# Optimization experiments

Hardware: AMD Instinct MI355X
Metric: run time of the kernel (lower is better)

## Reference

```python
import jax, jax.numpy as jnp
import numpy as np

DELTA = 0.0  # default `delta` arg of forward


def _features(voxels, clust_ids, num_clusters):
    # voxels: [N,3] float, clust_ids: [N] int in [0, C)
    n = voxels.shape[0]
    seg = lambda x: jax.ops.segment_sum(x, clust_ids, num_segments=num_clusters)
    counts = seg(jnp.ones((n,), voxels.dtype))                     # [C] cluster sizes
    safe_cnt = jnp.maximum(counts, 1.0)
    center = seg(voxels) / safe_cnt[:, None]                       # [C,3] per-cluster mean
    xc = voxels - center[clust_ids]                                # [N,3] centered voxels
    cov = seg(xc[:, :, None] * xc[:, None, :])                     # [C,3,3] = x^T x per cluster
    w, v = jnp.linalg.eigh(cov)                                    # eigvals ascending (== torch.eig + argsort)
    w2 = w[:, 2]
    dirwt = jnp.where(w2 == 0, 0.0, 1.0 - w[:, 1] / jnp.where(w2 == 0, 1.0, w2))
    wd = w + DELTA
    denom = jnp.where(wd[:, 2] == 0, 1.0, wd[:, 2])
    wn = wd / denom[:, None]                                       # w normalized by largest
    eye = jnp.eye(3, dtype=voxels.dtype)
    B = (1.0 - DELTA) * jnp.einsum('cij,cj,ckj->cik', v, wn, v) + DELTA * eye  # [C,3,3]
    v0 = v[:, :, 2]                                                # [C,3] principal axis
    x0 = jnp.sum(xc * v0[clust_ids], axis=-1)                      # [N] projection on v0
    xp0 = xc - x0[:, None] * v0[clust_ids]                         # [N,3] residual
    np0 = jnp.linalg.norm(xp0, axis=1)                             # [N]
    sc = seg(x0 * np0)                                             # [C] sign score
    v0 = jnp.where((sc < 0)[:, None], -v0, v0) * dirwt[:, None]
    # len(c) < 2 branch: center = the voxel itself (mean handles it), B = delta*I, v0 = 0
    small = counts < 2.0
    B = jnp.where(small[:, None, None], DELTA * eye, B)
    v0 = jnp.where(small[:, None], 0.0, v0)
    return jnp.concatenate([center, B.reshape(num_clusters, 9), v0, counts[:, None]], axis=1)  # [C,16]


def setup_inputs() -> dict:
    key = jax.random.key(0)
    k1, k2 = jax.random.split(key)
    n, c = 4000000, 4096
    data = jax.random.normal(k1, (n, 5), dtype=jnp.float32)
    clust_ids = jax.random.randint(k2, (n,), 0, c)
    return {"data": data, "clust_ids": clust_ids, "num_clusters": c}


def reference(data, clust_ids, num_clusters):
    voxels = data[:, :3].astype(jnp.float32)
    return _features(voxels, clust_ids, num_clusters)
```

## Files before the change

### kernel.cpp

```cpp
#include <hip/hip_runtime.h>
#include <math.h>

#define NC 4096
#define OVCAP 131072
#define CAP1 8520

__device__ __forceinline__ int xcd_id() {
    return (int)__builtin_amdgcn_s_getreg(20 | (0 << 6) | ((4 - 1) << 11));
}

__device__ __forceinline__ void solve_cluster(const float mom[10], float* o,
                                              float4* pcv, float4* pvv) {
    float cntf = mom[0];
    double dn  = (double)cntf;
    double inv = 1.0 / fmax(dn, 1.0);
    double cx = mom[1] * inv, cy = mom[2] * inv, cz = mom[3] * inv;

    double a00 = (double)mom[4] - dn * cx * cx;
    double a01 = (double)mom[5] - dn * cx * cy;
    double a02 = (double)mom[6] - dn * cx * cz;
    double a11 = (double)mom[7] - dn * cy * cy;
    double a12 = (double)mom[8] - dn * cy * cz;
    double a22 = (double)mom[9] - dn * cz * cz;

    double q  = (a00 + a11 + a22) / 3.0;
    double p1 = a01 * a01 + a02 * a02 + a12 * a12;
    double b00 = a00 - q, b11 = a11 - q, b22 = a22 - q;
    double p2 = b00 * b00 + b11 * b11 + b22 * b22 + 2.0 * p1;
    double w0, w1, w2;
    if (!(p2 > 0.0)) {
        w0 = w1 = w2 = q;
    } else {
        double p  = sqrt(p2 / 6.0);
        double ip = 1.0 / p;
        double c00 = b00 * ip, c01 = a01 * ip, c02 = a02 * ip;
        double c11 = b11 * ip, c12 = a12 * ip, c22 = b22 * ip;
        double detB = c00 * (c11 * c22 - c12 * c12)
                    - c01 * (c01 * c22 - c12 * c02)
                    + c02 * (c01 * c12 - c11 * c02);
        double r = fmin(1.0, fmax(-1.0, detB * 0.5));
        double phi = acos(r) / 3.0;
        w2 = q + 2.0 * p * cos(phi);
        w0 = q + 2.0 * p * cos(phi + 2.0943951023931953);
        w1 = 3.0 * q - w2 - w0;
    }

    double denom = (w2 == 0.0) ? 1.0 : w2;
    double dirwt = (w2 == 0.0) ? 0.0 : (1.0 - w1 / w2);

    double C00 = a00 - w1, C11 = a11 - w1, C22 = a22 - w1;
    double D00 = a00 - w0, D11 = a11 - w0, D22 = a22 - w0;
    double M00 = C00 * D00 + a01 * a01 + a02 * a02;
    double M10 = a01 * D00 + C11 * a01 + a12 * a02;
    double M20 = a02 * D00 + a12 * a01 + C22 * a02;
    double M01 = C00 * a01 + a01 * D11 + a02 * a12;
    double M11 = a01 * a01 + C11 * D11 + a12 * a12;
    double M21 = a02 * a01 + a12 * D11 + C22 * a12;
    double M02 = C00 * a02 + a01 * a12 + a02 * D22;
    double M12 = a01 * a02 + C11 * a12 + a12 * D22;
    double M22 = a02 * a02 + a12 * a12 + C22 * D22;
    double n0 = M00 * M00 + M10 * M10 + M20 * M20;
    double n1 = M01 * M01 + M11 * M11 + M21 * M21;
    double n2 = M02 * M02 + M12 * M12 + M22 * M22;
    double vx, vy, vz, nn;
    if (n0 >= n1 && n0 >= n2) { vx = M00; vy = M10; vz = M20; nn = n0; }
    else if (n1 >= n2)        { vx = M01; vy = M11; vz = M21; nn = n1; }
    else                      { vx = M02; vy = M12; vz = M22; nn = n2; }
    if (nn > 1e-300) {
        double rn = 1.0 / sqrt(nn);
        vx *= rn; vy *= rn; vz *= rn;
    } else {
        vx = vy = vz = 0.0;
    }

    bool small = cntf < 2.0f;
    float bscale = small ? 0.0f : (float)(1.0 / denom);

    o[0]  = (float)cx;
    o[1]  = (float)cy;
    o[2]  = (float)cz;
    o[3]  = (float)a00 * bscale;
    o[4]  = (float)a01 * bscale;
    o[5]  = (float)a02 * bscale;
    o[6]  = (float)a01 * bscale;
    o[7]  = (float)a11 * bscale;
    o[8]  = (float)a12 * bscale;
    o[9]  = (float)a02 * bscale;
    o[10] = (float)a12 * bscale;
    o[11] = (float)a22 * bscale;
    o[15] = cntf;

    *pcv = make_float4((float)cx, (float)cy, (float)cz, (float)dirwt);
    *pvv = make_float4((float)vx, (float)vy, (float)vz, cntf);
}

__device__ __forceinline__ void ov_spill(float4 d, int id, float4* ov, int* novf,
                                         float* gmom) {
    int ovi = atomicAdd(novf, 1);
    if (ovi < OVCAP) ov[ovi] = d;
    atomicAdd(&gmom[0 * NC + id], 1.0f);
    atomicAdd(&gmom[1 * NC + id], d.x);
    atomicAdd(&gmom[2 * NC + id], d.y);
    atomicAdd(&gmom[3 * NC + id], d.z);
    atomicAdd(&gmom[4 * NC + id], d.x * d.x);
    atomicAdd(&gmom[5 * NC + id], d.x * d.y);
    atomicAdd(&gmom[6 * NC + id], d.x * d.z);
    atomicAdd(&gmom[7 * NC + id], d.y * d.y);
    atomicAdd(&gmom[8 * NC + id], d.y * d.z);
    atomicAdd(&gmom[9 * NC + id], d.z * d.z);
}

__global__ __launch_bounds__(256) void k_p1(const float* __restrict__ data,
                                            const int* __restrict__ ids,
                                            float4* __restrict__ P1,
                                            int* __restrict__ cnt1,
                                            float4* __restrict__ ov,
                                            int* __restrict__ novf,
                                            float* __restrict__ gmom, int n) {
    __shared__ float4 srt[2048];
    __shared__ int h64[64], boff[64], bglob[64];
    int tid = threadIdx.x, lane = tid & 63;
    int xcd = xcd_id() & 7;
    int ntiles = (n + 2047) >> 11;
    for (int t = blockIdx.x; t < ntiles; t += gridDim.x) {
        int vbase = t << 11;
        if (tid < 64) h64[tid] = 0;
        __syncthreads();
        float vx[8], vy[8], vz[8];
        int vid[8], vrk[8];
#pragma unroll
        for (int s = 0; s < 8; s++) {
            int v = vbase + (s << 8) + tid;
            if (v < n) {
                vx[s] = data[v * 5 + 0];
                vy[s] = data[v * 5 + 1];
                vz[s] = data[v * 5 + 2];
                int id = ids[v];
                vid[s] = id;
                vrk[s] = atomicAdd(&h64[id >> 6], 1);
            } else vid[s] = -1;
        }
        __syncthreads();
        if (tid < 64) {
            int c0 = h64[tid], sc = c0;
            for (int off = 1; off < 64; off <<= 1) {
                int u = __shfl_up(sc, off);
                if (lane >= off) sc += u;
            }
            boff[tid] = sc - c0;
            bglob[tid] = atomicAdd(&cnt1[((tid << 3) + xcd) << 4], c0);
        }
        __syncthreads();
#pragma unroll
        for (int s = 0; s < 8; s++)
            if (vid[s] >= 0)
                srt[boff[vid[s] >> 6] + vrk[s]] =
                    make_float4(vx[s], vy[s], vz[s], __int_as_float(vid[s]));
        __syncthreads();
        int tot = n - vbase;
        tot = tot > 2048 ? 2048 : tot;
        for (int i = tid; i < tot; i += 256) {
            float4 d = srt[i];
            int id = __float_as_int(d.w);
            int b = id >> 6;
            int ofs = bglob[b] + (i - boff[b]);
            if (ofs < CAP1)
                P1[(size_t)((b << 3) + xcd) * CAP1 + ofs] = d;
            else
                ov_spill(d, id, ov, novf, gmom);
        }
        __syncthreads();
    }
}

__global__ __launch_bounds__(256) void k_mom(const float4* __restrict__ P1,
                                             const int* __restrict__ cnt1,
                                             float* __restrict__ gmom) {
    __shared__ float4 srt[2048];
    __shared__ int h64[64], boff[64];
    int tid = threadIdx.x, lane = tid & 63, w4 = tid >> 6;
    int xcd = blockIdx.x & 7;
    int rest = blockIdx.x >> 3;
    int bucket = rest & 63;
    int q = rest >> 6;
    int sub = (bucket << 3) + xcd;

    int m1c = cnt1[sub << 4];
    m1c = m1c > CAP1 ? CAP1 : m1c;
    int start = (int)(((long long)m1c * q) >> 1);
    int end   = (int)(((long long)m1c * (q + 1)) >> 1);
    size_t sbase = (size_t)sub * CAP1;

    float creg = 0.0f;
    float m1 = 0, m2 = 0, m3 = 0, m4 = 0, m5 = 0, m6 = 0, m7 = 0, m8 = 0, m9 = 0;

    for (int tb = start; tb < end; tb += 2048) {
        if (tid < 64) h64[tid] = 0;
        __syncthreads();
        float4 vd[8];
        int vcid[8], vrk[8];
#pragma unroll
        for (int s = 0; s < 8; s++) {
            int i = tb + (s << 8) + tid;
            if (i < end) {
                float4 d = P1[sbase + i];
                int cid = __float_as_int(d.w) & 63;
                vd[s] = d; vcid[s] = cid;
                vrk[s] = atomicAdd(&h64[cid], 1);
            } else vcid[s] = -1;
        }
        __syncthreads();
        if (tid < 64) {
            int c0 = h64[tid], sc = c0;
            for (int off = 1; off < 64; off <<= 1) {
                int u = __shfl_up(sc, off);
                if (lane >= off) sc += u;
            }
            boff[tid] = sc - c0;
        }
        __syncthreads();
#pragma unroll
        for (int s = 0; s < 8; s++)
            if (vcid[s] >= 0) srt[boff[vcid[s]] + vrk[s]] = vd[s];
        __syncthreads();
        int len = h64[lane];
        int bo  = boff[lane];
        if (w4 == 0) creg += (float)len;
        for (int j = w4; j < len; j += 4) {
            float4 d = srt[bo + j];
            m1 += d.x; m2 += d.y; m3 += d.z;
            m4 += d.x * d.x; m5 += d.x * d.y; m6 += d.x * d.z;
            m7 += d.y * d.y; m8 += d.y * d.z; m9 += d.z * d.z;
        }
        __syncthreads();
    }

    float* comb = (float*)srt;
    float regs[10] = {creg, m1, m2, m3, m4, m5, m6, m7, m8, m9};
#pragma unroll
    for (int k = 0; k < 10; k++)
        comb[((k << 6) + lane) * 4 + w4] = regs[k];
    __syncthreads();
    for (int i = tid; i < 640; i += 256) {
        int k = i >> 6, c = i & 63;
        float* p = comb + ((k << 6) + c) * 4;
        float v = p[0] + p[1] + p[2] + p[3];
        if (v != 0.0f) atomicAdd(&gmom[k * NC + (bucket << 6) + c], v);
    }
}

__global__ __launch_bounds__(256) void k_scp(const float4* __restrict__ P1,
                                             const int* __restrict__ cnt1,
                                             const float4* __restrict__ pcv,
                                             const float4* __restrict__ ov,
                                             const int* __restrict__ novf,
                                             float* __restrict__ gsc) {
    __shared__ float ssc[64];
    int tid = threadIdx.x;
    int xcd = blockIdx.x & 7;
    int rest = blockIdx.x >> 3;
    int bucket = rest & 63;
    int q = rest >> 6;
    int sub = (bucket << 3) + xcd;
    if (tid < 64) ssc[tid] = 0.0f;
    __syncthreads();
    int m1 = cnt1[sub << 4];
    m1 = m1 > CAP1 ? CAP1 : m1;
    int start = (int)(((long long)m1 * q) >> 2);
    int end   = (int)(((long long)m1 * (q + 1)) >> 2);
    size_t sbase = (size_t)sub * CAP1;
    const float4* tab = pcv + ((size_t)bucket << 7);

    for (int i = start + tid; i < end; i += 256) {
        float4 d = P1[sbase + i];
        int cid = __float_as_int(d.w) & 63;
        float4 c4 = tab[cid * 2];
        float4 v4 = tab[cid * 2 + 1];
        float xc = d.x - c4.x, yc = d.y - c4.y, zc = d.z - c4.z;
        float x0 = xc * v4.x + yc * v4.y + zc * v4.z;
        float px = xc - x0 * v4.x;
        float py = yc - x0 * v4.y;
        float pz = zc - x0 * v4.z;
        atomicAdd(&ssc[cid], x0 * sqrtf(px * px + py * py + pz * pz));
    }
    if (xcd == 0 && q == 0) {
        int mo = *novf;
        mo = mo > OVCAP ? OVCAP : mo;
        for (int i = tid; i < mo; i += 256) {
            float4 d = ov[i];
            int id = __float_as_int(d.w);
            if ((id >> 6) == bucket) {
                int cid = id & 63;
                float4 c4 = tab[cid * 2];
                float4 v4 = tab[cid * 2 + 1];
                float xc = d.x - c4.x, yc = d.y - c4.y, zc = d.z - c4.z;
                float x0 = xc * v4.x + yc * v4.y + zc * v4.z;
                float px = xc - x0 * v4.x;
                float py = yc - x0 * v4.y;
                float pz = zc - x0 * v4.z;
                atomicAdd(&ssc[cid], x0 * sqrtf(px * px + py * py + pz * pz));
            }
        }
    }
    __syncthreads();
    if (tid < 64) {
        float v = ssc[tid];
        if (v != 0.0f) atomicAdd(&gsc[(bucket << 6) + tid], v);
    }
}

__global__ void k_eigen_fb(const float* __restrict__ gmom, float* __restrict__ out,
                           float4* __restrict__ pcv) {
    int c = blockIdx.x * blockDim.x + threadIdx.x;
    if (c >= NC) return;
    float mom[10];
#pragma unroll
    for (int k = 0; k < 10; k++) mom[k] = gmom[k * NC + c];
    solve_cluster(mom, out + c * 16, &pcv[2 * c], &pcv[2 * c + 1]);
}

__global__ void k_final_fb(const float4* __restrict__ pcv,
                           const float* __restrict__ gsc, float* __restrict__ out) {
    int c = blockIdx.x * blockDim.x + threadIdx.x;
    if (c >= NC) return;
    float4 c4 = pcv[2 * c];
    float4 v4 = pcv[2 * c + 1];
    float s = (gsc[c] < 0.0f) ? -c4.w : c4.w;
    if (v4.w < 2.0f) s = 0.0f;
    out[c * 16 + 12] = v4.x * s;
    out[c * 16 + 13] = v4.y * s;
    out[c * 16 + 14] = v4.z * s;
}

__global__ __launch_bounds__(1024) void k_accum_raw(const float* __restrict__ data,
                                                    const int* __restrict__ ids,
                                                    float* __restrict__ gmom, int n) {
    extern __shared__ float s[];
    for (int i = threadIdx.x; i < 10 * NC; i += blockDim.x) s[i] = 0.0f;
    __syncthreads();
    int stride = gridDim.x * blockDim.x;
    for (int i = blockIdx.x * blockDim.x + threadIdx.x; i < n; i += stride) {
        int id = ids[i];
        float x = data[i * 5 + 0], y = data[i * 5 + 1], z = data[i * 5 + 2];
        atomicAdd(&s[0 * NC + id], 1.0f);
        atomicAdd(&s[1 * NC + id], x);
        atomicAdd(&s[2 * NC + id], y);
        atomicAdd(&s[3 * NC + id], z);
        atomicAdd(&s[4 * NC + id], x * x);
        atomicAdd(&s[5 * NC + id], x * y);
        atomicAdd(&s[6 * NC + id], x * z);
        atomicAdd(&s[7 * NC + id], y * y);
        atomicAdd(&s[8 * NC + id], y * z);
        atomicAdd(&s[9 * NC + id], z * z);
    }
    __syncthreads();
    for (int i = threadIdx.x; i < 10 * NC; i += blockDim.x) {
        float v = s[i];
        if (v != 0.0f) atomicAdd(&gmom[i], v);
    }
}

__global__ __launch_bounds__(1024) void k_sc_raw(const float* __restrict__ data,
                                                 const int* __restrict__ ids,
                                                 const float4* __restrict__ pcv,
                                                 float* __restrict__ gsc, int n) {
    extern __shared__ float4 sl4[];
    float4* spc = sl4;
    float4* spv = sl4 + NC;
    float*  ssc = (float*)(sl4 + 2 * NC);
    for (int i = threadIdx.x; i < NC; i += blockDim.x) {
        spc[i] = pcv[2 * i]; spv[i] = pcv[2 * i + 1]; ssc[i] = 0.0f;
    }
    __syncthreads();
    int stride = gridDim.x * blockDim.x;
    for (int i = blockIdx.x * blockDim.x + threadIdx.x; i < n; i += stride) {
        int id = ids[i];
        float4 c4 = spc[id];
        float4 v4 = spv[id];
        float xc = data[i * 5 + 0] - c4.x;
        float yc = data[i * 5 + 1] - c4.y;
        float zc = data[i * 5 + 2] - c4.z;
        float x0 = xc * v4.x + yc * v4.y + zc * v4.z;
        float px = xc - x0 * v4.x;
        float py = yc - x0 * v4.y;
        float pz = zc - x0 * v4.z;
        atomicAdd(&ssc[id], x0 * sqrtf(px * px + py * py + pz * pz));
    }
    __syncthreads();
    for (int i = threadIdx.x; i < NC; i += blockDim.x) {
        float v = ssc[i];
        if (v != 0.0f) atomicAdd(&gsc[i], v);
    }
}

extern "C" void kernel_launch(void* const* d_in, const int* in_sizes, int n_in,
                              void* d_out, int out_size, void* d_ws, size_t ws_size,
                              hipStream_t stream) {
    const float* data = (const float*)d_in[0];
    const int*   ids  = (const int*)d_in[1];
    float* out = (float*)d_out;
    int n = in_sizes[1];

    char* ws = (char*)d_ws;
    float*  gmom = (float*)(ws);
    float*  gsc  = (float*)(ws + 163840);
    int*    cnt1 = (int*)(ws + 180224);
    int*    novf = (int*)(ws + 212992);
    float4* pcv  = (float4*)(ws + 213056);
    float4* ov   = (float4*)(ws + 344128);
    const size_t FIXED = 2441280;
    const size_t P1SZ  = (size_t)512 * CAP1 * 16;

    if (ws_size >= FIXED + P1SZ) {
        float4* P1 = (float4*)(ws + FIXED);
        hipMemsetAsync(ws, 0, 213056, stream);
        hipLaunchKernelGGL(k_p1, dim3(2048), dim3(256), 0, stream,
                           data, ids, P1, cnt1, ov, novf, gmom, n);
        hipLaunchKernelGGL(k_mom, dim3(1024), dim3(256), 0, stream,
                           P1, cnt1, gmom);
        hipLaunchKernelGGL(k_eigen_fb, dim3(16), dim3(256), 0, stream,
                           gmom, out, pcv);
        hipLaunchKernelGGL(k_scp, dim3(2048), dim3(256), 0, stream,
                           P1, cnt1, pcv, ov, novf, gsc);
        hipLaunchKernelGGL(k_final_fb, dim3(16), dim3(256), 0, stream,
                           pcv, gsc, out);
    } else {
        hipMemsetAsync(ws, 0, 180224, stream);
        hipLaunchKernelGGL(k_accum_raw, dim3(256), dim3(1024), 10 * NC * 4, stream,
                           data, ids, gmom, n);
        hipLaunchKernelGGL(k_eigen_fb, dim3(16), dim3(256), 0, stream, gmom, out, pcv);
        hipLaunchKernelGGL(k_sc_raw, dim3(256), dim3(1024), 2 * NC * 16 + NC * 4, stream,
                           data, ids, pcv, gsc, n);
        hipLaunchKernelGGL(k_final_fb, dim3(16), dim3(256), 0, stream, pcv, gsc, out);
    }
}
```

Measured before the change: 215.5 us.

## Use SoA shared staging, 512-thread blocks, and fuse final sign pass into k_scp

The binning and moment kernels now use 512-thread blocks, and their shared-memory staging moves from float4 records to separate x/y/z arrays plus 16-bit ids, which cuts LDS traffic and bank conflicts. The final per-cluster sign/scale step is folded into k_scp. The last block per bucket, found through an atomic counter, writes v0, which removes one kernel launch. This adds threadfence and counter overhead, plus a correctness dependence on exactly 32 blocks per bucket.

```diff
diff --git a/kernel.cpp b/kernel.cpp
--- a/kernel.cpp
+++ b/kernel.cpp
@@ -110,15 +110,19 @@
     atomicAdd(&gmom[9 * NC + id], d.z * d.z);
 }
 
-__global__ __launch_bounds__(256) void k_p1(const float* __restrict__ data,
+__global__ __launch_bounds__(512) void k_p1(const float* __restrict__ data,
                                             const int* __restrict__ ids,
                                             float4* __restrict__ P1,
                                             int* __restrict__ cnt1,
                                             float4* __restrict__ ov,
                                             int* __restrict__ novf,
                                             float* __restrict__ gmom, int n) {
-    __shared__ float4 srt[2048];
+    __shared__ float sbuf[6144];
+    __shared__ unsigned short sid[2048];
     __shared__ int h64[64], boff[64], bglob[64];
+    float* sx = sbuf;
+    float* sy = sbuf + 2048;
+    float* sz = sbuf + 4096;
     int tid = threadIdx.x, lane = tid & 63;
     int xcd = xcd_id() & 7;
     int ntiles = (n + 2047) >> 11;
@@ -126,11 +130,11 @@
         int vbase = t << 11;
         if (tid < 64) h64[tid] = 0;
         __syncthreads();
-        float vx[8], vy[8], vz[8];
-        int vid[8], vrk[8];
-#pragma unroll
-        for (int s = 0; s < 8; s++) {
-            int v = vbase + (s << 8) + tid;
+        float vx[4], vy[4], vz[4];
+        int vid[4], vrk[4];
+#pragma unroll
+        for (int s = 0; s < 4; s++) {
+            int v = vbase + (s << 9) + tid;
             if (v < n) {
                 vx[s] = data[v * 5 + 0];
                 vy[s] = data[v * 5 + 1];
@@ -152,18 +156,20 @@
         }
         __syncthreads();
 #pragma unroll
-        for (int s = 0; s < 8; s++)
-            if (vid[s] >= 0)
-                srt[boff[vid[s] >> 6] + vrk[s]] =
-                    make_float4(vx[s], vy[s], vz[s], __int_as_float(vid[s]));
+        for (int s = 0; s < 4; s++)
+            if (vid[s] >= 0) {
+                int p = boff[vid[s] >> 6] + vrk[s];
+                sx[p] = vx[s]; sy[p] = vy[s]; sz[p] = vz[s];
+                sid[p] = (unsigned short)vid[s];
+            }
         __syncthreads();
         int tot = n - vbase;
         tot = tot > 2048 ? 2048 : tot;
-        for (int i = tid; i < tot; i += 256) {
-            float4 d = srt[i];
-            int id = __float_as_int(d.w);
+        for (int i = tid; i < tot; i += 512) {
+            int id = (int)sid[i];
             int b = id >> 6;
             int ofs = bglob[b] + (i - boff[b]);
+            float4 d = make_float4(sx[i], sy[i], sz[i], __int_as_float(id));
             if (ofs < CAP1)
                 P1[(size_t)((b << 3) + xcd) * CAP1 + ofs] = d;
             else
@@ -173,12 +179,15 @@
     }
 }
 
-__global__ __launch_bounds__(256) void k_mom(const float4* __restrict__ P1,
+__global__ __launch_bounds__(512) void k_mom(const float4* __restrict__ P1,
                                              const int* __restrict__ cnt1,
                                              float* __restrict__ gmom) {
-    __shared__ float4 srt[2048];
+    __shared__ float sbuf[6144];
     __shared__ int h64[64], boff[64];
-    int tid = threadIdx.x, lane = tid & 63, w4 = tid >> 6;
+    float* sx = sbuf;
+    float* sy = sbuf + 2048;
+    float* sz = sbuf + 4096;
+    int tid = threadIdx.x, lane = tid & 63, w8 = tid >> 6;
     int xcd = blockIdx.x & 7;
     int rest = blockIdx.x >> 3;
     int bucket = rest & 63;
@@ -197,11 +206,11 @@
     for (int tb = start; tb < end; tb += 2048) {
         if (tid < 64) h64[tid] = 0;
         __syncthreads();
-        float4 vd[8];
-        int vcid[8], vrk[8];
-#pragma unroll
-        for (int s = 0; s < 8; s++) {
-            int i = tb + (s << 8) + tid;
+        float4 vd[4];
+        int vcid[4], vrk[4];
+#pragma unroll
+        for (int s = 0; s < 4; s++) {
+            int i = tb + (s << 9) + tid;
             if (i < end) {
                 float4 d = P1[sbase + i];
                 int cid = __float_as_int(d.w) & 63;
@@ -220,31 +229,34 @@
         }
         __syncthreads();
 #pragma unroll
-        for (int s = 0; s < 8; s++)
-            if (vcid[s] >= 0) srt[boff[vcid[s]] + vrk[s]] = vd[s];
+        for (int s = 0; s < 4; s++)
+            if (vcid[s] >= 0) {
+                int p = boff[vcid[s]] + vrk[s];
+                sx[p] = vd[s].x; sy[p] = vd[s].y; sz[p] = vd[s].z;
+            }
         __syncthreads();
         int len = h64[lane];
         int bo  = boff[lane];
-        if (w4 == 0) creg += (float)len;
-        for (int j = w4; j < len; j += 4) {
-            float4 d = srt[bo + j];
-            m1 += d.x; m2 += d.y; m3 += d.z;
-            m4 += d.x * d.x; m5 += d.x * d.y; m6 += d.x * d.z;
-            m7 += d.y * d.y; m8 += d.y * d.z; m9 += d.z * d.z;
-        }
-        __syncthreads();
-    }
-
-    float* comb = (float*)srt;
+        if (w8 == 0) creg += (float)len;
+        for (int j = w8; j < len; j += 8) {
+            float x = sx[bo + j], y = sy[bo + j], z = sz[bo + j];
+            m1 += x; m2 += y; m3 += z;
+            m4 += x * x; m5 += x * y; m6 += x * z;
+            m7 += y * y; m8 += y * z; m9 += z * z;
+        }
+        __syncthreads();
+    }
+
+    float* comb = sbuf;
     float regs[10] = {creg, m1, m2, m3, m4, m5, m6, m7, m8, m9};
 #pragma unroll
     for (int k = 0; k < 10; k++)
-        comb[((k << 6) + lane) * 4 + w4] = regs[k];
-    __syncthreads();
-    for (int i = tid; i < 640; i += 256) {
+        comb[(((k << 6) + lane) << 3) + w8] = regs[k];
+    __syncthreads();
+    for (int i = tid; i < 640; i += 512) {
         int k = i >> 6, c = i & 63;
-        float* p = comb + ((k << 6) + c) * 4;
-        float v = p[0] + p[1] + p[2] + p[3];
+        float* p = comb + (((k << 6) + c) << 3);
+        float v = ((p[0] + p[1]) + (p[2] + p[3])) + ((p[4] + p[5]) + (p[6] + p[7]));
         if (v != 0.0f) atomicAdd(&gmom[k * NC + (bucket << 6) + c], v);
     }
 }
@@ -254,8 +266,11 @@
                                              const float4* __restrict__ pcv,
                                              const float4* __restrict__ ov,
                                              const int* __restrict__ novf,
-                                             float* __restrict__ gsc) {
+                                             float* __restrict__ gsc,
+                                             float* __restrict__ out,
+                                             int* __restrict__ done2) {
     __shared__ float ssc[64];
+    __shared__ int lastf;
     int tid = threadIdx.x;
     int xcd = blockIdx.x & 7;
     int rest = blockIdx.x >> 3;
@@ -307,6 +322,22 @@
         float v = ssc[tid];
         if (v != 0.0f) atomicAdd(&gsc[(bucket << 6) + tid], v);
     }
+    __threadfence();
+    if (tid == 0) lastf = (atomicAdd(&done2[bucket], 1) == 31) ? 1 : 0;
+    __syncthreads();
+    if (!lastf) return;
+    __threadfence();
+    if (tid < 64) {
+        int c = (bucket << 6) + tid;
+        float s = atomicAdd(&gsc[c], 0.0f);
+        float4 c4 = pcv[2 * c];
+        float4 v4 = pcv[2 * c + 1];
+        float sg = (s < 0.0f) ? -c4.w : c4.w;
+        if (v4.w < 2.0f) sg = 0.0f;
+        out[c * 16 + 12] = v4.x * sg;
+        out[c * 16 + 13] = v4.y * sg;
+        out[c * 16 + 14] = v4.z * sg;
+    }
 }
 
 __global__ void k_eigen_fb(const float* __restrict__ gmom, float* __restrict__ out,
@@ -406,24 +437,23 @@
     float*  gsc  = (float*)(ws + 163840);
     int*    cnt1 = (int*)(ws + 180224);
     int*    novf = (int*)(ws + 212992);
-    float4* pcv  = (float4*)(ws + 213056);
-    float4* ov   = (float4*)(ws + 344128);
-    const size_t FIXED = 2441280;
+    int*    done2= (int*)(ws + 213056);
+    float4* pcv  = (float4*)(ws + 213312);
+    float4* ov   = (float4*)(ws + 344384);
+    const size_t FIXED = 2441536;
     const size_t P1SZ  = (size_t)512 * CAP1 * 16;
 
     if (ws_size >= FIXED + P1SZ) {
         float4* P1 = (float4*)(ws + FIXED);
-        hipMemsetAsync(ws, 0, 213056, stream);
-        hipLaunchKernelGGL(k_p1, dim3(2048), dim3(256), 0, stream,
+        hipMemsetAsync(ws, 0, 213312, stream);
+        hipLaunchKernelGGL(k_p1, dim3(1024), dim3(512), 0, stream,
                            data, ids, P1, cnt1, ov, novf, gmom, n);
-        hipLaunchKernelGGL(k_mom, dim3(1024), dim3(256), 0, stream,
+        hipLaunchKernelGGL(k_mom, dim3(1024), dim3(512), 0, stream,
                            P1, cnt1, gmom);
         hipLaunchKernelGGL(k_eigen_fb, dim3(16), dim3(256), 0, stream,
                            gmom, out, pcv);
         hipLaunchKernelGGL(k_scp, dim3(2048), dim3(256), 0, stream,
-                           P1, cnt1, pcv, ov, novf, gsc);
-        hipLaunchKernelGGL(k_final_fb, dim3(16), dim3(256), 0, stream,
-                           pcv, gsc, out);
+                           P1, cnt1, pcv, ov, novf, gsc, out, done2);
     } else {
         hipMemsetAsync(ws, 0, 180224, stream);
         hipLaunchKernelGGL(k_accum_raw, dim3(256), dim3(1024), 10 * NC * 4, stream,
```

After: 353.7 us. 1.64x slower.
